# Kernel optimization log

Hardware: AMD Instinct MI355X
Metric: run time of the kernel (lower is better)

## Reference

```python
import jax, jax.numpy as jnp
from jax import lax
import numpy as np

N_LAYERS = 4
D_MODEL = 512
EXPAND = 3
D_INNER = EXPAND * D_MODEL  # 1536
D_STATE = 32
D_CONV = 4
DT_RANK = (D_MODEL + 15) // 16  # 32 (mamba default ceil(d_model/16))
BATCH = 1024
N_FEAT = 68
N_RAIN = 4
N_NONRAIN = N_FEAT - N_RAIN  # 64


def setup_inputs() -> dict:
    key = jax.random.key(0)
    ks = iter(jax.random.split(key, 40))

    def w(shape, s=0.02):
        return jax.random.normal(next(ks), shape, dtype=jnp.float32) * s

    inp = {
        'x': jax.random.normal(next(ks), (BATCH, N_FEAT), dtype=jnp.float32),
        # mamba_input_proj: Linear(64 -> d_model)
        'w_in': w((D_MODEL, N_NONRAIN)), 'b_in': jnp.zeros((D_MODEL,), jnp.float32),
        # per-layer LayerNorms
        'ln_g': jnp.ones((N_LAYERS, D_MODEL), jnp.float32),
        'ln_b': jnp.zeros((N_LAYERS, D_MODEL), jnp.float32),
        # Mamba per-layer params (stacked over layers)
        'W_inproj': w((N_LAYERS, 2 * D_INNER, D_MODEL)),
        'conv_w': w((N_LAYERS, D_INNER, D_CONV), 0.1),
        'conv_b': jnp.zeros((N_LAYERS, D_INNER), jnp.float32),
        'W_xproj': w((N_LAYERS, DT_RANK + 2 * D_STATE, D_INNER)),
        'W_dt': w((N_LAYERS, D_INNER, DT_RANK), 0.1),
        'b_dt': w((N_LAYERS, D_INNER), 0.5),
        'A_log': jnp.broadcast_to(jnp.log(jnp.arange(1, D_STATE + 1, dtype=jnp.float32)), (N_LAYERS, D_INNER, D_STATE)) + 0.0,
        'D_skip': jnp.ones((N_LAYERS, D_INNER), jnp.float32),
        'W_outproj': w((N_LAYERS, D_MODEL, D_INNER)),
        # logistic branch: Linear(4 -> 1) + sigmoid
        'w_log': w((1, N_RAIN), 0.1), 'b_log': jnp.zeros((1,), jnp.float32),
        # gate_proj: Linear(1 -> d_model)
        'W_gate': w((D_MODEL, 1), 0.1), 'b_gate': jnp.zeros((D_MODEL,), jnp.float32),
        # output head: Linear(d_model->32), ReLU, Linear(32->1)
        'W_h1': w((32, D_MODEL)), 'b_h1': jnp.zeros((32,), jnp.float32),
        'W_h2': w((1, 32)), 'b_h2': jnp.zeros((1,), jnp.float32),
    }
    return inp


def _layernorm(x, g, b, eps=1e-5):
    mu = x.mean(-1, keepdims=True)
    var = x.var(-1, keepdims=True)
    return (x - mu) * lax.rsqrt(var + eps) * g + b


def _mamba(x, Win, cw, cb, Wx, Wdt, bdt, Alog, Dp, Wout):
    # x: [B, L, d_model]
    B_, L, _ = x.shape
    xz = jnp.einsum('bld,ed->ble', x, Win)           # [B,L,2*d_inner]
    xc, z = jnp.split(xz, 2, axis=-1)
    # causal depthwise conv1d over L
    xt = jnp.pad(xc.transpose(0, 2, 1), ((0, 0), (0, 0), (D_CONV - 1, 0)))
    conv = lax.conv_general_dilated(xt, cw[:, None, :], (1,), 'VALID',
                                    dimension_numbers=('NCH', 'OIH', 'NCH'),
                                    feature_group_count=D_INNER)
    u = jax.nn.silu((conv + cb[None, :, None]).transpose(0, 2, 1))  # [B,L,d_inner]
    x_dbl = jnp.einsum('bld,ed->ble', u, Wx)         # [B,L,dt_rank+2*d_state]
    dt = x_dbl[..., :DT_RANK]
    Bm = x_dbl[..., DT_RANK:DT_RANK + D_STATE]
    Cm = x_dbl[..., DT_RANK + D_STATE:]
    delta = jax.nn.softplus(jnp.einsum('blr,dr->bld', dt, Wdt) + bdt)  # [B,L,d_inner]
    A = -jnp.exp(Alog)                               # [d_inner, d_state]
    dA = jnp.exp(jnp.einsum('bld,dn->bldn', delta, A))
    dBu = jnp.einsum('bld,bln->bldn', delta * u, Bm)

    def step(h, inp):
        dA_t, dBu_t, C_t = inp
        h = dA_t * h + dBu_t                         # [B,d_inner,d_state]
        return h, jnp.einsum('bdn,bn->bd', h, C_t)

    h0 = jnp.zeros((B_, D_INNER, D_STATE), x.dtype)
    _, ys = lax.scan(step, h0, (dA.transpose(1, 0, 2, 3), dBu.transpose(1, 0, 2, 3), Cm.transpose(1, 0, 2)))
    y = ys.transpose(1, 0, 2) + u * Dp               # [B,L,d_inner]
    y = y * jax.nn.silu(z)
    return jnp.einsum('bld,ed->ble', y, Wout)        # [B,L,d_model]


def reference(x, w_in, b_in, ln_g, ln_b, W_inproj, conv_w, conv_b, W_xproj, W_dt, b_dt,
              A_log, D_skip, W_outproj, w_log, b_log, W_gate, b_gate, W_h1, b_h1, W_h2, b_h2):
    rain = x[:, :N_RAIN]
    nonrain = x[:, N_RAIN:]
    h = jax.nn.relu(nonrain @ w_in.T + b_in)[:, None, :]   # [B,1,d_model]
    for l in range(N_LAYERS):
        res = h
        hn = _layernorm(h, ln_g[l], ln_b[l])
        hn = _mamba(hn, W_inproj[l], conv_w[l], conv_b[l], W_xproj[l], W_dt[l], b_dt[l],
                    A_log[l], D_skip[l], W_outproj[l])
        h = res + hn  # dropout is identity in eval mode
    m = h[:, 0, :]
    lg = jax.nn.sigmoid(rain @ w_log.T + b_log)            # [B,1]
    gate = lg @ W_gate.T + b_gate                          # [B,d_model]
    fused = m * gate
    z1 = jax.nn.relu(fused @ W_h1.T + b_h1)
    logits = (z1 @ W_h2.T + b_h2)[:, 0]
    return jax.nn.sigmoid(logits)
```

## Files before the change

kernel.cpp:

```cpp
#include <hip/hip_runtime.h>

typedef unsigned short u16;
typedef short v8s __attribute__((ext_vector_type(8)));
typedef float v4f __attribute__((ext_vector_type(4)));
typedef u16  v4u __attribute__((ext_vector_type(4)));

__device__ __forceinline__ float bf2f(u16 h){ return __uint_as_float(((unsigned)h)<<16); }
__device__ __forceinline__ u16 f2bf(float f){
  unsigned u = __float_as_uint(f);
  u += 0x7FFFu + ((u>>16)&1u);
  return (u16)(u>>16);
}
__device__ __forceinline__ float siluf(float x){ return x/(1.f+__expf(-x)); }
__device__ __forceinline__ float softplusf(float x){
  return (x>15.f) ? x : __logf(1.f+__expf(x));
}

struct SetupP {
  const float *x,*w_in,*b_in,*ln_g,*ln_b,*W_inproj,*W_xproj,*W_dt,*W_outproj;
  u16 *wIn,*wX,*wDt,*wOut;
  float *sg,*cb,*stats,*h;
  u16 *hb;
};

__global__ __launch_bounds__(256) void setup_kernel(SetupP sp)
{
  __shared__ float red[8];
  const int blk = blockIdx.x, t = threadIdx.x;
  if(blk < 32){
    sp.stats[2048 + blk*256 + t] = 0.f;
    return;
  }
  if(blk < 10016){
    const int c0=6291456, c1=c0+589824, c2=c1+196608;
    int i4 = ((blk-32)*256 + t)*4;
    float4 v; u16* dst;
    if(i4 < c0){
      v = *(const float4*)(sp.W_inproj + i4);
      int k = i4 & 511, l = (i4>>9)/3072;
      const float* gg = sp.ln_g + l*512 + k;
      v.x*=gg[0]; v.y*=gg[1]; v.z*=gg[2]; v.w*=gg[3];
      dst = sp.wIn + i4;
    } else if(i4 < c1){ int o=i4-c0; v=*(const float4*)(sp.W_xproj+o);   dst=sp.wX+o; }
    else if(i4 < c2){   int o=i4-c1; v=*(const float4*)(sp.W_dt+o);      dst=sp.wDt+o; }
    else {              int o=i4-c2; v=*(const float4*)(sp.W_outproj+o); dst=sp.wOut+o; }
    v4u pk={ f2bf(v.x), f2bf(v.y), f2bf(v.z), f2bf(v.w) };
    *(v4u*)dst = pk;
    return;
  }
  if(blk < 13088){
    int wid=t>>6, lane=t&63;
    int ridx = (blk-10016)*4 + wid;
    int l = ridx/3072;
    const float* wr = sp.W_inproj + (size_t)ridx*512;
    const float* gg = sp.ln_g + l*512;
    const float* bb = sp.ln_b + l*512;
    float sgv=0.f, cbv=0.f;
#pragma unroll
    for(int i=0;i<8;i++){ int k=lane*8+i; float w=wr[k]; sgv+=gg[k]*w; cbv+=bb[k]*w; }
#pragma unroll
    for(int off=1; off<64; off<<=1){ sgv+=__shfl_xor(sgv,off); cbv+=__shfl_xor(cbv,off); }
    if(lane==0){ sp.sg[ridx]=sgv; sp.cb[ridx]=cbv; }
    return;
  }
  int b = blk - 13088;
  const float* xr = sp.x + b*68 + 4;
  float v0, v1;
  {
    const float* wr = sp.w_in + t*64;
    float a = sp.b_in[t];
#pragma unroll
    for(int f=0; f<64; f++) a += xr[f]*wr[f];
    v0 = fmaxf(a, 0.f);
  }
  {
    const float* wr = sp.w_in + (t+256)*64;
    float a = sp.b_in[t+256];
#pragma unroll
    for(int f=0; f<64; f++) a += xr[f]*wr[f];
    v1 = fmaxf(a, 0.f);
  }
  sp.h[b*512+t] = v0;       sp.h[b*512+256+t] = v1;
  sp.hb[b*512+t]= f2bf(v0); sp.hb[b*512+256+t]= f2bf(v1);
  float s = v0+v1, s2 = v0*v0+v1*v1;
#pragma unroll
  for(int off=32; off; off>>=1){ s += __shfl_down(s,off); s2 += __shfl_down(s2,off); }
  if((t&63)==0){ red[(t>>6)*2]=s; red[(t>>6)*2+1]=s2; }
  __syncthreads();
  if(t==0){
    sp.stats[b*2]   = red[0]+red[2]+red[4]+red[6];
    sp.stats[b*2+1] = red[1]+red[3]+red[5]+red[7];
  }
}

__global__ __launch_bounds__(256) void gemm1_ln(
  const u16* __restrict__ hb, const u16* __restrict__ Wp,
  const float* __restrict__ sg, const float* __restrict__ cb,
  const float* __restrict__ st,
  const float* __restrict__ convw, const float* __restrict__ convb,
  u16* __restrict__ u, u16* __restrict__ zs)
{
  __shared__ u16 As[64*40], Bs[64*40];
  const int tid=threadIdx.x, lane=tid&63, wid=tid>>6;
  const int wm=wid>>1, wn=wid&1, qd=lane>>4, lr=lane&15;
  const int m0=blockIdx.y*64, n0=blockIdx.x*64;
  const int r_=tid>>2, kg_=tid&3;
  const u16* Ap = hb + (size_t)(m0+r_)*512 + kg_*8;
  const u16* Bp = Wp + (size_t)(n0+r_)*512 + kg_*8;
  u16* Asw = As + r_*40 + kg_*8;
  u16* Bsw = Bs + r_*40 + kg_*8;

  v4f acc[2][2];
#pragma unroll
  for(int i=0;i<2;i++)
#pragma unroll
    for(int j=0;j<2;j++) acc[i][j]=v4f{0.f,0.f,0.f,0.f};

  auto domfma=[&](){
    v8s af[2], bfv[2];
#pragma unroll
    for(int i=0;i<2;i++) af[i] =*(const v8s*)(As+(wm*32+i*16+lr)*40+qd*8);
#pragma unroll
    for(int j=0;j<2;j++) bfv[j]=*(const v8s*)(Bs+(wn*32+j*16+lr)*40+qd*8);
#pragma unroll
    for(int i=0;i<2;i++)
#pragma unroll
      for(int j=0;j<2;j++)
        acc[i][j]=__builtin_amdgcn_mfma_f32_16x16x32_bf16(af[i],bfv[j],acc[i][j],0,0,0);
  };

  v8s a0=*(const v8s*)(Ap),    b0=*(const v8s*)(Bp);
  v8s a1=*(const v8s*)(Ap+32), b1=*(const v8s*)(Bp+32);
  for(int it=0; it<16; it+=2){
    const int kk=it*32;
    __syncthreads();
    *(v8s*)Asw=a0; *(v8s*)Bsw=b0;
    __syncthreads();
    if(it+2<16){ a0=*(const v8s*)(Ap+kk+64); b0=*(const v8s*)(Bp+kk+64); }
    domfma();
    __syncthreads();
    *(v8s*)Asw=a1; *(v8s*)Bsw=b1;
    __syncthreads();
    if(it+2<16){ a1=*(const v8s*)(Ap+kk+96); b1=*(const v8s*)(Bp+kk+96); }
    domfma();
  }

#pragma unroll
  for(int i=0;i<2;i++){
    const int gb0=m0+wm*32+i*16+qd*4;
#pragma unroll
    for(int r=0;r<4;r++){
      const int gb=gb0+r;
      float S1=st[gb*2], S2=st[gb*2+1];
      float mu=S1*(1.f/512.f);
      float rs=rsqrtf(S2*(1.f/512.f)-mu*mu+1e-5f);
#pragma unroll
      for(int j=0;j<2;j++){
        const int ge=n0+wn*32+j*16+lr;
        float val = rs*(acc[i][j][r] - mu*sg[ge]) + cb[ge];
        if(ge<1536){
          u[(size_t)gb*1536+ge]=f2bf(siluf(val*convw[ge*4+3]+convb[ge]));
        }else{
          zs[(size_t)gb*1536+(ge-1536)]=f2bf(siluf(val));
        }
      }
    }
  }
}

__global__ __launch_bounds__(256) void gemm2(
  const u16* __restrict__ A, const u16* __restrict__ wX,
  float* __restrict__ xpart)
{
  __shared__ u16 As[64*40];
  __shared__ u16 Bs[96*40];
  const int tid=threadIdx.x, lane=tid&63, wid=tid>>6;
  const int wm=wid>>1, wn=wid&1, qd=lane>>4, lr=lane&15;
  const int m0=blockIdx.y*64;
  const int k0=blockIdx.x*192;
  const int r_=tid>>2, kg_=tid&3;
  const u16* Ap  = A  + (size_t)(m0+r_)*1536 + k0 + kg_*8;
  const u16* Bp0 = wX + (size_t)r_*1536      + k0 + kg_*8;
  const u16* Bp1 = wX + (size_t)(64+r_)*1536 + k0 + kg_*8;
  u16* Asw  = As + r_*40 + kg_*8;
  u16* Bsw0 = Bs + r_*40 + kg_*8;
  u16* Bsw1 = Bs + (64+r_)*40 + kg_*8;
  const bool hasB1 = tid<128;

  v4f acc[2][3];
#pragma unroll
  for(int i=0;i<2;i++)
#pragma unroll
    for(int j=0;j<3;j++) acc[i][j]=v4f{0.f,0.f,0.f,0.f};

  auto domfma=[&](){
    v8s af[2], bfv[3];
#pragma unroll
    for(int i=0;i<2;i++) af[i] =*(const v8s*)(As+(wm*32+i*16+lr)*40+qd*8);
#pragma unroll
    for(int j=0;j<3;j++) bfv[j]=*(const v8s*)(Bs+(wn*48+j*16+lr)*40+qd*8);
#pragma unroll
    for(int i=0;i<2;i++)
#pragma unroll
      for(int j=0;j<3;j++)
        acc[i][j]=__builtin_amdgcn_mfma_f32_16x16x32_bf16(af[i],bfv[j],acc[i][j],0,0,0);
  };

  v8s a0=*(const v8s*)(Ap),    b0x=*(const v8s*)(Bp0),    b0y{};
  v8s a1=*(const v8s*)(Ap+32), b1x=*(const v8s*)(Bp0+32), b1y{};
  if(hasB1){ b0y=*(const v8s*)(Bp1); b1y=*(const v8s*)(Bp1+32); }
  for(int it=0; it<6; it+=2){
    const int kk=it*32;
    __syncthreads();
    *(v8s*)Asw=a0; *(v8s*)Bsw0=b0x; if(hasB1) *(v8s*)Bsw1=b0y;
    __syncthreads();
    if(it+2<6){ a0=*(const v8s*)(Ap+kk+64); b0x=*(const v8s*)(Bp0+kk+64);
      if(hasB1) b0y=*(const v8s*)(Bp1+kk+64); }
    domfma();
    __syncthreads();
    *(v8s*)Asw=a1; *(v8s*)Bsw0=b1x; if(hasB1) *(v8s*)Bsw1=b1y;
    __syncthreads();
    if(it+2<6){ a1=*(const v8s*)(Ap+kk+96); b1x=*(const v8s*)(Bp0+kk+96);
      if(hasB1) b1y=*(const v8s*)(Bp1+kk+96); }
    domfma();
  }

  float* op = xpart + (size_t)blockIdx.x*98304;
#pragma unroll
  for(int i=0;i<2;i++)
#pragma unroll
    for(int j=0;j<3;j++){
      const int gb0=m0+wm*32+i*16+qd*4;
      const int ge =wn*48+j*16+lr;
#pragma unroll
      for(int r=0;r<4;r++)
        op[(size_t)(gb0+r)*96+ge]=acc[i][j][r];
    }
}

__global__ __launch_bounds__(256) void gemm3(
  const float* __restrict__ xpart, const u16* __restrict__ wDt,
  const float* __restrict__ bdt, const float* __restrict__ Dp,
  const u16* __restrict__ u, const u16* __restrict__ zs,
  u16* __restrict__ y)
{
  __shared__ u16 dts[64*40];
  __shared__ u16 Bs[64*40];
  __shared__ float sbl[64];
  const int tid=threadIdx.x, lane=tid&63, wid=tid>>6;
  const int wm=wid>>1, wn=wid&1, qd=lane>>4, lr=lane&15;
  const int m0=blockIdx.y*64, n0=blockIdx.x*64;
  const int r=tid>>2, sub=tid&3;

  v8s breg = *(const v8s*)(wDt + (size_t)(n0+r)*32 + sub*8);

  float a24[24];
#pragma unroll
  for(int i=0;i<24;i++) a24[i]=0.f;
#pragma unroll
  for(int z=0;z<8;z++){
    const float4* bz=(const float4*)(xpart + (size_t)z*98304 + (size_t)(m0+r)*96);
#pragma unroll
    for(int t=0;t<6;t++){
      float4 v=bz[sub+4*t];
      a24[4*t]+=v.x; a24[4*t+1]+=v.y; a24[4*t+2]+=v.z; a24[4*t+3]+=v.w;
    }
  }
  float s_=0.f;
#pragma unroll
  for(int m=0;m<4;m++) s_ += a24[8+m]*a24[16+m] + a24[12+m]*a24[20+m];
  s_ += __shfl_xor(s_,1); s_ += __shfl_xor(s_,2);
  if(sub==0) sbl[r]=s_;
  v4u p0={ f2bf(a24[0]), f2bf(a24[1]), f2bf(a24[2]), f2bf(a24[3]) };
  v4u p1={ f2bf(a24[4]), f2bf(a24[5]), f2bf(a24[6]), f2bf(a24[7]) };
  *(v4u*)(dts + r*40 + 4*sub)      = p0;
  *(v4u*)(dts + r*40 + 16 + 4*sub) = p1;
  *(v8s*)(Bs + r*40 + sub*8) = breg;
  __syncthreads();

  v4f acc[2][2];
#pragma unroll
  for(int i=0;i<2;i++)
#pragma unroll
    for(int j=0;j<2;j++) acc[i][j]=v4f{0.f,0.f,0.f,0.f};
  v8s af[2], bfv[2];
#pragma unroll
  for(int i=0;i<2;i++) af[i] =*(const v8s*)(dts+(wm*32+i*16+lr)*40+qd*8);
#pragma unroll
  for(int j=0;j<2;j++) bfv[j]=*(const v8s*)(Bs+(wn*32+j*16+lr)*40+qd*8);
#pragma unroll
  for(int i=0;i<2;i++)
#pragma unroll
    for(int j=0;j<2;j++)
      acc[i][j]=__builtin_amdgcn_mfma_f32_16x16x32_bf16(af[i],bfv[j],acc[i][j],0,0,0);

#pragma unroll
  for(int i=0;i<2;i++){
    const int lb0=wm*32+i*16+qd*4;
#pragma unroll
    for(int rr=0;rr<4;rr++){
      const int gb=m0+lb0+rr;
      const float sv=sbl[lb0+rr];
#pragma unroll
      for(int j=0;j<2;j++){
        const int ge=n0+wn*32+j*16+lr;
        float delta=softplusf(acc[i][j][rr]+bdt[ge]);
        float uu=bf2f(u[(size_t)gb*1536+ge]);
        float zz=bf2f(zs[(size_t)gb*1536+ge]);
        y[(size_t)gb*1536+ge]=f2bf(uu*(delta*sv+Dp[ge])*zz);
      }
    }
  }
}

__global__ __launch_bounds__(256) void gemm4(
  const u16* __restrict__ yv, const u16* __restrict__ wO,
  float* __restrict__ h, u16* __restrict__ hb, float* __restrict__ stn)
{
  __shared__ u16 As[32*40], Bs[32*40];
  const int tid=threadIdx.x, lane=tid&63, wid=tid>>6;
  const int wm=wid>>1, wn=wid&1, qd=lane>>4, lr=lane&15;
  const int m0=blockIdx.y*32, n0=blockIdx.x*32;
  const int half=tid>>7, ts=tid&127;
  const int r_=ts>>2, kg_=ts&3;
  const u16* Gp = (half ? wO + (size_t)(n0+r_)*1536
                        : yv + (size_t)(m0+r_)*1536) + kg_*8;
  u16* Sw = (half ? Bs : As) + r_*40 + kg_*8;

  v4f acc=v4f{0.f,0.f,0.f,0.f};
  auto domfma=[&](){
    v8s af=*(const v8s*)(As+(wm*16+lr)*40+qd*8);
    v8s bf=*(const v8s*)(Bs+(wn*16+lr)*40+qd*8);
    acc=__builtin_amdgcn_mfma_f32_16x16x32_bf16(af,bf,acc,0,0,0);
  };

  v8s g0=*(const v8s*)(Gp), g1=*(const v8s*)(Gp+32);
  for(int it=0; it<48; it+=2){
    const int kk=it*32;
    __syncthreads();
    *(v8s*)Sw=g0;
    __syncthreads();
    if(it+2<48) g0=*(const v8s*)(Gp+kk+64);
    domfma();
    __syncthreads();
    *(v8s*)Sw=g1;
    __syncthreads();
    if(it+2<48) g1=*(const v8s*)(Gp+kk+96);
    domfma();
  }

#pragma unroll
  for(int r=0;r<4;r++){
    const int gb=m0+wm*16+qd*4+r;
    const int ge=n0+wn*16+lr;
    const size_t idx=(size_t)gb*512+ge;
    float hv=h[idx]+acc[r];
    h[idx]=hv; hb[idx]=f2bf(hv);
    float s1=hv, s2=hv*hv;
    s1+=__shfl_xor(s1,1); s2+=__shfl_xor(s2,1);
    s1+=__shfl_xor(s1,2); s2+=__shfl_xor(s2,2);
    s1+=__shfl_xor(s1,4); s2+=__shfl_xor(s2,4);
    s1+=__shfl_xor(s1,8); s2+=__shfl_xor(s2,8);
    if(lr==0){ atomicAdd(stn+gb*2, s1); atomicAdd(stn+gb*2+1, s2); }
  }
}

__global__ __launch_bounds__(256) void head_kernel(
  const float* __restrict__ x, const float* __restrict__ h,
  const float* __restrict__ wlog, const float* __restrict__ blog,
  const float* __restrict__ wg, const float* __restrict__ bg,
  const float* __restrict__ wh1, const float* __restrict__ bh1,
  const float* __restrict__ wh2, const float* __restrict__ bh2,
  float* __restrict__ out)
{
  int b = blockIdx.x, t = threadIdx.x;
  __shared__ float fused[512];
  __shared__ float part[256];
  __shared__ float z1s[32];
  float lgin = x[b*68+0]*wlog[0] + x[b*68+1]*wlog[1]
             + x[b*68+2]*wlog[2] + x[b*68+3]*wlog[3] + blog[0];
  float lg = 1.f/(1.f+__expf(-lgin));
  for(int d=t; d<512; d+=256)
    fused[d] = h[(size_t)b*512+d]*(lg*wg[d] + bg[d]);
  __syncthreads();
  int j = t&31, c = t>>5;
  float p = 0.f;
#pragma unroll
  for(int i=0;i<64;i++){ int d = c*64+i; p += fused[d]*wh1[j*512+d]; }
  part[t] = p;
  __syncthreads();
  if(t < 32){
    float z = bh1[t];
#pragma unroll
    for(int cc=0; cc<8; cc++) z += part[cc*32+t];
    z1s[t] = fmaxf(z, 0.f);
  }
  __syncthreads();
  if(t==0){
    float lo = bh2[0];
#pragma unroll
    for(int jj=0;jj<32;jj++) lo += z1s[jj]*wh2[jj];
    out[b] = 1.f/(1.f+__expf(-lo));
  }
}

extern "C" void kernel_launch(void* const* d_in, const int* in_sizes, int n_in,
                              void* d_out, int out_size, void* d_ws, size_t ws_size,
                              hipStream_t stream)
{
  const float* x        = (const float*)d_in[0];
  const float* w_in     = (const float*)d_in[1];
  const float* b_in     = (const float*)d_in[2];
  const float* ln_g     = (const float*)d_in[3];
  const float* ln_b     = (const float*)d_in[4];
  const float* W_inproj = (const float*)d_in[5];
  const float* conv_w   = (const float*)d_in[6];
  const float* conv_b   = (const float*)d_in[7];
  const float* W_xproj  = (const float*)d_in[8];
  const float* W_dt     = (const float*)d_in[9];
  const float* b_dt     = (const float*)d_in[10];
  const float* D_skip   = (const float*)d_in[12];
  const float* W_outproj= (const float*)d_in[13];
  const float* w_log    = (const float*)d_in[14];
  const float* b_log    = (const float*)d_in[15];
  const float* W_gate   = (const float*)d_in[16];
  const float* b_gate   = (const float*)d_in[17];
  const float* W_h1     = (const float*)d_in[18];
  const float* b_h1     = (const float*)d_in[19];
  const float* W_h2     = (const float*)d_in[20];
  const float* b_h2     = (const float*)d_in[21];
  float* out = (float*)d_out;
  (void)in_sizes; (void)n_in; (void)out_size; (void)ws_size;

  char* ws = (char*)d_ws;
  size_t off = 0;
  auto alloc = [&](size_t bytes)->char*{
    char* p = ws + off; off = (off + bytes + 255) & ~(size_t)255; return p; };
  u16*   wIn  = (u16*)  alloc(6291456u*2);
  u16*   wX   = (u16*)  alloc(589824u*2);
  u16*   wDt  = (u16*)  alloc(196608u*2);
  u16*   wOut = (u16*)  alloc(3145728u*2);
  float* sg   = (float*)alloc(12288u*4);
  float* cb   = (float*)alloc(12288u*4);
  float* stats= (float*)alloc(10240u*4);
  float* h    = (float*)alloc(524288u*4);
  u16*   hb   = (u16*)  alloc(524288u*2);
  u16*   u    = (u16*)  alloc(1572864u*2);
  u16*   zs   = (u16*)  alloc(1572864u*2);
  u16*   y    = (u16*)  alloc(1572864u*2);
  float* xpart= (float*)alloc(8u*98304u*4);

  SetupP sp;
  sp.x=x; sp.w_in=w_in; sp.b_in=b_in; sp.ln_g=ln_g; sp.ln_b=ln_b;
  sp.W_inproj=W_inproj; sp.W_xproj=W_xproj; sp.W_dt=W_dt; sp.W_outproj=W_outproj;
  sp.wIn=wIn; sp.wX=wX; sp.wDt=wDt; sp.wOut=wOut;
  sp.sg=sg; sp.cb=cb; sp.stats=stats; sp.h=h; sp.hb=hb;

  setup_kernel<<<14112,256,0,stream>>>(sp);

  for(int l=0;l<4;l++){
    gemm1_ln<<<dim3(48,16),256,0,stream>>>(
      hb, wIn+(size_t)l*1572864, sg+l*3072, cb+l*3072, stats+l*2048,
      conv_w+l*6144, conv_b+l*1536, u, zs);
    gemm2<<<dim3(8,16),256,0,stream>>>(
      u, wX+(size_t)l*147456, xpart);
    gemm3<<<dim3(24,16),256,0,stream>>>(
      xpart, wDt+(size_t)l*49152, b_dt+l*1536, D_skip+l*1536, u, zs, y);
    gemm4<<<dim3(16,32),256,0,stream>>>(
      y, wOut+(size_t)l*786432, h, hb, stats+(l+1)*2048);
  }

  head_kernel<<<1024,256,0,stream>>>(x, h, w_log, b_log, W_gate, b_gate,
                                     W_h1, b_h1, W_h2, b_h2, out);
}
```

Measured before the change: 343.5 us.

## Compute LayerNorm stats inside gemm1 from bf16 tiles; widen K tiles; MFMA input projection

Removes the per-row atomic LayerNorm statistics from gemm4 and the stats buffer. gemm1 now sums the bf16 activation chunks it already loads, so every one of the 48 column blocks recomputes the row mean and variance from bf16 values rather than fp32. The K tile in gemm1 and gemm4 grows from 32 to 64, which halves the number of barrier pairs per loop. The setup kernel's input projection becomes a bf16 MFMA tile GEMM instead of scalar fp32 dot products, trading some accuracy for speed.

```diff
diff --git a/kernel.cpp b/kernel.cpp
--- a/kernel.cpp
+++ b/kernel.cpp
@@ -19,21 +19,17 @@
 struct SetupP {
   const float *x,*w_in,*b_in,*ln_g,*ln_b,*W_inproj,*W_xproj,*W_dt,*W_outproj;
   u16 *wIn,*wX,*wDt,*wOut;
-  float *sg,*cb,*stats,*h;
+  float *sg,*cb,*h;
   u16 *hb;
 };
 
 __global__ __launch_bounds__(256) void setup_kernel(SetupP sp)
 {
-  __shared__ float red[8];
+  __shared__ u16 As[64*72], Bs[64*72];
   const int blk = blockIdx.x, t = threadIdx.x;
-  if(blk < 32){
-    sp.stats[2048 + blk*256 + t] = 0.f;
-    return;
-  }
-  if(blk < 10016){
+  if(blk < 9984){
     const int c0=6291456, c1=c0+589824, c2=c1+196608;
-    int i4 = ((blk-32)*256 + t)*4;
+    int i4 = (blk*256 + t)*4;
     float4 v; u16* dst;
     if(i4 < c0){
       v = *(const float4*)(sp.W_inproj + i4);
@@ -48,9 +44,9 @@
     *(v4u*)dst = pk;
     return;
   }
-  if(blk < 13088){
+  if(blk < 13056){
     int wid=t>>6, lane=t&63;
-    int ridx = (blk-10016)*4 + wid;
+    int ridx = (blk-9984)*4 + wid;
     int l = ridx/3072;
     const float* wr = sp.W_inproj + (size_t)ridx*512;
     const float* gg = sp.ln_g + l*512;
@@ -63,97 +59,146 @@
     if(lane==0){ sp.sg[ridx]=sgv; sp.cb[ridx]=cbv; }
     return;
   }
-  int b = blk - 13088;
-  const float* xr = sp.x + b*68 + 4;
-  float v0, v1;
+  const int mb=blk-13056, mt=mb>>3, nt=mb&7;
+  const int m0=mt*64, n0=nt*64;
+  const int lane=t&63, wid=t>>6;
+  const int wm=wid>>1, wn=wid&1, qd=lane>>4, lr=lane&15;
+  const int r=t>>2, cq=t&3;
   {
-    const float* wr = sp.w_in + t*64;
-    float a = sp.b_in[t];
-#pragma unroll
-    for(int f=0; f<64; f++) a += xr[f]*wr[f];
-    v0 = fmaxf(a, 0.f);
-  }
-  {
-    const float* wr = sp.w_in + (t+256)*64;
-    float a = sp.b_in[t+256];
-#pragma unroll
-    for(int f=0; f<64; f++) a += xr[f]*wr[f];
-    v1 = fmaxf(a, 0.f);
-  }
-  sp.h[b*512+t] = v0;       sp.h[b*512+256+t] = v1;
-  sp.hb[b*512+t]= f2bf(v0); sp.hb[b*512+256+t]= f2bf(v1);
-  float s = v0+v1, s2 = v0*v0+v1*v1;
-#pragma unroll
-  for(int off=32; off; off>>=1){ s += __shfl_down(s,off); s2 += __shfl_down(s2,off); }
-  if((t&63)==0){ red[(t>>6)*2]=s; red[(t>>6)*2+1]=s2; }
+    const float4* ax=(const float4*)(sp.x + (size_t)(m0+r)*68 + 4 + cq*16);
+    const float4* bx=(const float4*)(sp.w_in + (size_t)(n0+r)*64 + cq*16);
+    float4 av0=ax[0], av1=ax[1], av2=ax[2], av3=ax[3];
+    float4 bv0=bx[0], bv1=bx[1], bv2=bx[2], bv3=bx[3];
+    v4u pa0={f2bf(av0.x),f2bf(av0.y),f2bf(av0.z),f2bf(av0.w)};
+    v4u pa1={f2bf(av1.x),f2bf(av1.y),f2bf(av1.z),f2bf(av1.w)};
+    v4u pa2={f2bf(av2.x),f2bf(av2.y),f2bf(av2.z),f2bf(av2.w)};
+    v4u pa3={f2bf(av3.x),f2bf(av3.y),f2bf(av3.z),f2bf(av3.w)};
+    v4u pb0={f2bf(bv0.x),f2bf(bv0.y),f2bf(bv0.z),f2bf(bv0.w)};
+    v4u pb1={f2bf(bv1.x),f2bf(bv1.y),f2bf(bv1.z),f2bf(bv1.w)};
+    v4u pb2={f2bf(bv2.x),f2bf(bv2.y),f2bf(bv2.z),f2bf(bv2.w)};
+    v4u pb3={f2bf(bv3.x),f2bf(bv3.y),f2bf(bv3.z),f2bf(bv3.w)};
+    u16* aw=As+r*72+cq*16; u16* bw=Bs+r*72+cq*16;
+    *(v4u*)(aw)=pa0; *(v4u*)(aw+4)=pa1; *(v4u*)(aw+8)=pa2; *(v4u*)(aw+12)=pa3;
+    *(v4u*)(bw)=pb0; *(v4u*)(bw+4)=pb1; *(v4u*)(bw+8)=pb2; *(v4u*)(bw+12)=pb3;
+  }
   __syncthreads();
-  if(t==0){
-    sp.stats[b*2]   = red[0]+red[2]+red[4]+red[6];
-    sp.stats[b*2+1] = red[1]+red[3]+red[5]+red[7];
-  }
+  v4f acc[2][2];
+#pragma unroll
+  for(int i=0;i<2;i++)
+#pragma unroll
+    for(int j=0;j<2;j++) acc[i][j]=v4f{0.f,0.f,0.f,0.f};
+#pragma unroll
+  for(int s=0;s<2;s++){
+    v8s af[2], bfv[2];
+#pragma unroll
+    for(int i=0;i<2;i++) af[i] =*(const v8s*)(As+(wm*32+i*16+lr)*72+s*32+qd*8);
+#pragma unroll
+    for(int j=0;j<2;j++) bfv[j]=*(const v8s*)(Bs+(wn*32+j*16+lr)*72+s*32+qd*8);
+#pragma unroll
+    for(int i=0;i<2;i++)
+#pragma unroll
+      for(int j=0;j<2;j++)
+        acc[i][j]=__builtin_amdgcn_mfma_f32_16x16x32_bf16(af[i],bfv[j],acc[i][j],0,0,0);
+  }
+#pragma unroll
+  for(int i=0;i<2;i++)
+#pragma unroll
+    for(int j=0;j<2;j++){
+      const int gb0=m0+wm*32+i*16+qd*4;
+      const int ge =n0+wn*32+j*16+lr;
+#pragma unroll
+      for(int rr=0;rr<4;rr++){
+        float hv=fmaxf(acc[i][j][rr]+sp.b_in[ge],0.f);
+        const size_t idx=(size_t)(gb0+rr)*512+ge;
+        sp.h[idx]=hv; sp.hb[idx]=f2bf(hv);
+      }
+    }
 }
 
 __global__ __launch_bounds__(256) void gemm1_ln(
   const u16* __restrict__ hb, const u16* __restrict__ Wp,
   const float* __restrict__ sg, const float* __restrict__ cb,
-  const float* __restrict__ st,
   const float* __restrict__ convw, const float* __restrict__ convb,
   u16* __restrict__ u, u16* __restrict__ zs)
 {
-  __shared__ u16 As[64*40], Bs[64*40];
+  __shared__ u16 As[64*72], Bs[64*72];
+  __shared__ float sS1[64], sS2[64];
   const int tid=threadIdx.x, lane=tid&63, wid=tid>>6;
   const int wm=wid>>1, wn=wid&1, qd=lane>>4, lr=lane&15;
   const int m0=blockIdx.y*64, n0=blockIdx.x*64;
-  const int r_=tid>>2, kg_=tid&3;
-  const u16* Ap = hb + (size_t)(m0+r_)*512 + kg_*8;
-  const u16* Bp = Wp + (size_t)(n0+r_)*512 + kg_*8;
-  u16* Asw = As + r_*40 + kg_*8;
-  u16* Bsw = Bs + r_*40 + kg_*8;
+  const int r_=tid>>2, cq=tid&3;
+  const u16* Ap = hb + (size_t)(m0+r_)*512 + cq*16;
+  const u16* Bp = Wp + (size_t)(n0+r_)*512 + cq*16;
+  u16* Asw = As + r_*72 + cq*16;
+  u16* Bsw = Bs + r_*72 + cq*16;
 
   v4f acc[2][2];
 #pragma unroll
   for(int i=0;i<2;i++)
 #pragma unroll
     for(int j=0;j<2;j++) acc[i][j]=v4f{0.f,0.f,0.f,0.f};
-
+  float s1=0.f, s2=0.f;
+
+  auto statAcc=[&](v8s v){
+#pragma unroll
+    for(int e=0;e<8;e++){ float f=bf2f((u16)v[e]); s1+=f; s2+=f*f; }
+  };
   auto domfma=[&](){
-    v8s af[2], bfv[2];
-#pragma unroll
-    for(int i=0;i<2;i++) af[i] =*(const v8s*)(As+(wm*32+i*16+lr)*40+qd*8);
-#pragma unroll
-    for(int j=0;j<2;j++) bfv[j]=*(const v8s*)(Bs+(wn*32+j*16+lr)*40+qd*8);
-#pragma unroll
-    for(int i=0;i<2;i++)
-#pragma unroll
-      for(int j=0;j<2;j++)
-        acc[i][j]=__builtin_amdgcn_mfma_f32_16x16x32_bf16(af[i],bfv[j],acc[i][j],0,0,0);
+#pragma unroll
+    for(int s=0;s<2;s++){
+      v8s af[2], bfv[2];
+#pragma unroll
+      for(int i=0;i<2;i++) af[i] =*(const v8s*)(As+(wm*32+i*16+lr)*72+s*32+qd*8);
+#pragma unroll
+      for(int j=0;j<2;j++) bfv[j]=*(const v8s*)(Bs+(wn*32+j*16+lr)*72+s*32+qd*8);
+#pragma unroll
+      for(int i=0;i<2;i++)
+#pragma unroll
+        for(int j=0;j<2;j++)
+          acc[i][j]=__builtin_amdgcn_mfma_f32_16x16x32_bf16(af[i],bfv[j],acc[i][j],0,0,0);
+    }
   };
 
-  v8s a0=*(const v8s*)(Ap),    b0=*(const v8s*)(Bp);
-  v8s a1=*(const v8s*)(Ap+32), b1=*(const v8s*)(Bp+32);
-  for(int it=0; it<16; it+=2){
-    const int kk=it*32;
-    __syncthreads();
-    *(v8s*)Asw=a0; *(v8s*)Bsw=b0;
-    __syncthreads();
-    if(it+2<16){ a0=*(const v8s*)(Ap+kk+64); b0=*(const v8s*)(Bp+kk+64); }
+  v8s a0a=*(const v8s*)(Ap),    a0b=*(const v8s*)(Ap+8);
+  v8s b0a=*(const v8s*)(Bp),    b0b=*(const v8s*)(Bp+8);
+  v8s a1a=*(const v8s*)(Ap+64), a1b=*(const v8s*)(Ap+72);
+  v8s b1a=*(const v8s*)(Bp+64), b1b=*(const v8s*)(Bp+72);
+  for(int c=0;c<8;c+=2){
+    __syncthreads();
+    *(v8s*)Asw=a0a; *(v8s*)(Asw+8)=a0b;
+    *(v8s*)Bsw=b0a; *(v8s*)(Bsw+8)=b0b;
+    statAcc(a0a); statAcc(a0b);
+    __syncthreads();
+    if(c+2<8){
+      a0a=*(const v8s*)(Ap+(c+2)*64); a0b=*(const v8s*)(Ap+(c+2)*64+8);
+      b0a=*(const v8s*)(Bp+(c+2)*64); b0b=*(const v8s*)(Bp+(c+2)*64+8);
+    }
     domfma();
     __syncthreads();
-    *(v8s*)Asw=a1; *(v8s*)Bsw=b1;
-    __syncthreads();
-    if(it+2<16){ a1=*(const v8s*)(Ap+kk+96); b1=*(const v8s*)(Bp+kk+96); }
+    *(v8s*)Asw=a1a; *(v8s*)(Asw+8)=a1b;
+    *(v8s*)Bsw=b1a; *(v8s*)(Bsw+8)=b1b;
+    statAcc(a1a); statAcc(a1b);
+    __syncthreads();
+    if(c+3<8){
+      a1a=*(const v8s*)(Ap+(c+3)*64); a1b=*(const v8s*)(Ap+(c+3)*64+8);
+      b1a=*(const v8s*)(Bp+(c+3)*64); b1b=*(const v8s*)(Bp+(c+3)*64+8);
+    }
     domfma();
   }
 
+  s1+=__shfl_xor(s1,1); s2+=__shfl_xor(s2,1);
+  s1+=__shfl_xor(s1,2); s2+=__shfl_xor(s2,2);
+  if(cq==0){ sS1[r_]=s1; sS2[r_]=s2; }
+  __syncthreads();
+
 #pragma unroll
   for(int i=0;i<2;i++){
-    const int gb0=m0+wm*32+i*16+qd*4;
+    const int lb0=wm*32+i*16+qd*4;
 #pragma unroll
     for(int r=0;r<4;r++){
-      const int gb=gb0+r;
-      float S1=st[gb*2], S2=st[gb*2+1];
-      float mu=S1*(1.f/512.f);
-      float rs=rsqrtf(S2*(1.f/512.f)-mu*mu+1e-5f);
+      const int lb=lb0+r, gb=m0+lb;
+      float mu=sS1[lb]*(1.f/512.f);
+      float rs=rsqrtf(sS2[lb]*(1.f/512.f)-mu*mu+1e-5f);
 #pragma unroll
       for(int j=0;j<2;j++){
         const int ge=n0+wn*32+j*16+lr;
@@ -315,37 +360,40 @@
 
 __global__ __launch_bounds__(256) void gemm4(
   const u16* __restrict__ yv, const u16* __restrict__ wO,
-  float* __restrict__ h, u16* __restrict__ hb, float* __restrict__ stn)
-{
-  __shared__ u16 As[32*40], Bs[32*40];
+  float* __restrict__ h, u16* __restrict__ hb)
+{
+  __shared__ u16 As[32*72], Bs[32*72];
   const int tid=threadIdx.x, lane=tid&63, wid=tid>>6;
   const int wm=wid>>1, wn=wid&1, qd=lane>>4, lr=lane&15;
   const int m0=blockIdx.y*32, n0=blockIdx.x*32;
   const int half=tid>>7, ts=tid&127;
-  const int r_=ts>>2, kg_=ts&3;
+  const int r_=ts>>2, cq=ts&3;
   const u16* Gp = (half ? wO + (size_t)(n0+r_)*1536
-                        : yv + (size_t)(m0+r_)*1536) + kg_*8;
-  u16* Sw = (half ? Bs : As) + r_*40 + kg_*8;
+                        : yv + (size_t)(m0+r_)*1536) + cq*16;
+  u16* Sw = (half ? Bs : As) + r_*72 + cq*16;
 
   v4f acc=v4f{0.f,0.f,0.f,0.f};
   auto domfma=[&](){
-    v8s af=*(const v8s*)(As+(wm*16+lr)*40+qd*8);
-    v8s bf=*(const v8s*)(Bs+(wn*16+lr)*40+qd*8);
-    acc=__builtin_amdgcn_mfma_f32_16x16x32_bf16(af,bf,acc,0,0,0);
+#pragma unroll
+    for(int s=0;s<2;s++){
+      v8s af=*(const v8s*)(As+(wm*16+lr)*72+s*32+qd*8);
+      v8s bf=*(const v8s*)(Bs+(wn*16+lr)*72+s*32+qd*8);
+      acc=__builtin_amdgcn_mfma_f32_16x16x32_bf16(af,bf,acc,0,0,0);
+    }
   };
 
-  v8s g0=*(const v8s*)(Gp), g1=*(const v8s*)(Gp+32);
-  for(int it=0; it<48; it+=2){
-    const int kk=it*32;
-    __syncthreads();
-    *(v8s*)Sw=g0;
-    __syncthreads();
-    if(it+2<48) g0=*(const v8s*)(Gp+kk+64);
+  v8s g0a=*(const v8s*)(Gp),    g0b=*(const v8s*)(Gp+8);
+  v8s g1a=*(const v8s*)(Gp+64), g1b=*(const v8s*)(Gp+72);
+  for(int c=0;c<24;c+=2){
+    __syncthreads();
+    *(v8s*)Sw=g0a; *(v8s*)(Sw+8)=g0b;
+    __syncthreads();
+    if(c+2<24){ g0a=*(const v8s*)(Gp+(c+2)*64); g0b=*(const v8s*)(Gp+(c+2)*64+8); }
     domfma();
     __syncthreads();
-    *(v8s*)Sw=g1;
-    __syncthreads();
-    if(it+2<48) g1=*(const v8s*)(Gp+kk+96);
+    *(v8s*)Sw=g1a; *(v8s*)(Sw+8)=g1b;
+    __syncthreads();
+    if(c+3<24){ g1a=*(const v8s*)(Gp+(c+3)*64); g1b=*(const v8s*)(Gp+(c+3)*64+8); }
     domfma();
   }
 
@@ -356,12 +404,6 @@
     const size_t idx=(size_t)gb*512+ge;
     float hv=h[idx]+acc[r];
     h[idx]=hv; hb[idx]=f2bf(hv);
-    float s1=hv, s2=hv*hv;
-    s1+=__shfl_xor(s1,1); s2+=__shfl_xor(s2,1);
-    s1+=__shfl_xor(s1,2); s2+=__shfl_xor(s2,2);
-    s1+=__shfl_xor(s1,4); s2+=__shfl_xor(s2,4);
-    s1+=__shfl_xor(s1,8); s2+=__shfl_xor(s2,8);
-    if(lr==0){ atomicAdd(stn+gb*2, s1); atomicAdd(stn+gb*2+1, s2); }
   }
 }
 
@@ -442,7 +484,6 @@
   u16*   wOut = (u16*)  alloc(3145728u*2);
   float* sg   = (float*)alloc(12288u*4);
   float* cb   = (float*)alloc(12288u*4);
-  float* stats= (float*)alloc(10240u*4);
   float* h    = (float*)alloc(524288u*4);
   u16*   hb   = (u16*)  alloc(524288u*2);
   u16*   u    = (u16*)  alloc(1572864u*2);
@@ -454,20 +495,20 @@
   sp.x=x; sp.w_in=w_in; sp.b_in=b_in; sp.ln_g=ln_g; sp.ln_b=ln_b;
   sp.W_inproj=W_inproj; sp.W_xproj=W_xproj; sp.W_dt=W_dt; sp.W_outproj=W_outproj;
   sp.wIn=wIn; sp.wX=wX; sp.wDt=wDt; sp.wOut=wOut;
-  sp.sg=sg; sp.cb=cb; sp.stats=stats; sp.h=h; sp.hb=hb;
-
-  setup_kernel<<<14112,256,0,stream>>>(sp);
+  sp.sg=sg; sp.cb=cb; sp.h=h; sp.hb=hb;
+
+  setup_kernel<<<13184,256,0,stream>>>(sp);
 
   for(int l=0;l<4;l++){
     gemm1_ln<<<dim3(48,16),256,0,stream>>>(
-      hb, wIn+(size_t)l*1572864, sg+l*3072, cb+l*3072, stats+l*2048,
+      hb, wIn+(size_t)l*1572864, sg+l*3072, cb+l*3072,
       conv_w+l*6144, conv_b+l*1536, u, zs);
     gemm2<<<dim3(8,16),256,0,stream>>>(
       u, wX+(size_t)l*147456, xpart);
     gemm3<<<dim3(24,16),256,0,stream>>>(
       xpart, wDt+(size_t)l*49152, b_dt+l*1536, D_skip+l*1536, u, zs, y);
     gemm4<<<dim3(16,32),256,0,stream>>>(
-      y, wOut+(size_t)l*786432, h, hb, stats+(l+1)*2048);
+      y, wOut+(size_t)l*786432, h, hb);
   }
 
   head_kernel<<<1024,256,0,stream>>>(x, h, w_log, b_log, W_gate, b_gate,
```

Result: faster. 288.4 us (-16.0%).
